# Kernel optimization log

Measured on AMD Instinct MI355X. Metric: run time of the kernel, lower is better.

The kernel has to match this reference:

```python
import jax, jax.numpy as jnp
import numpy as np

B, N, S, F = 16, 512, 7, 256
HID, NUM_CLASSES = 1024, 81
FLAT = S * S * F  # 12544


def setup_inputs() -> dict:
    key = jax.random.key(0)
    ks = jax.random.split(key, 8)
    features = jax.random.normal(ks[0], (B, N, S, S, F), dtype=jnp.float32)
    valid_mask = jax.random.randint(ks[1], (B, N), 0, 2) > 0
    W1 = jax.random.normal(ks[2], (FLAT, HID), dtype=jnp.float32) * (1.0 / np.sqrt(FLAT))
    b1 = jnp.zeros((HID,), dtype=jnp.float32)
    W2 = jax.random.normal(ks[3], (HID, HID), dtype=jnp.float32) * (1.0 / np.sqrt(HID))
    b2 = jnp.zeros((HID,), dtype=jnp.float32)
    W3 = jax.random.normal(ks[4], (HID, NUM_CLASSES), dtype=jnp.float32) * (1.0 / np.sqrt(HID))
    b3 = jnp.zeros((NUM_CLASSES,), dtype=jnp.float32)
    return {"features": features, "valid_mask": valid_mask, "W1": W1, "b1": b1,
            "W2": W2, "b2": b2, "W3": W3, "b3": b3, "features_size_pred": N}


def reference(features, valid_mask, W1, b1, W2, b2, W3, b3, features_size_pred):
    # The TF module masks out invalid ROIs, runs the MLP, then scatters results
    # back to original positions (pad + argsort + gather) with zeros for invalid
    # rows. That is mathematically identical to running the MLP on all ROIs and
    # zeroing invalid rows, which is the efficient dense form.
    b, n = features.shape[0], features.shape[1]
    x = features.reshape(b * n, FLAT)                      # [B*N, 12544]
    h = jax.nn.relu(x @ W1 + b1)                           # [B*N, HID]
    h = jax.nn.relu(h @ W2 + b2)                           # [B*N, HID]
    logits = (h @ W3 + b3).reshape(b, n, NUM_CLASSES)      # [B, N, C]
    mask = valid_mask.astype(logits.dtype)[..., None]      # [B, N, 1]
    return logits * mask
```

## Files before the change

### kernel.cpp

```cpp
#include <hip/hip_runtime.h>
#include <stdint.h>

#define DEVINL __device__ __forceinline__

typedef __bf16 bf16x8 __attribute__((ext_vector_type(8)));
typedef float f32x4 __attribute__((ext_vector_type(4)));

DEVINL unsigned short f32_to_bf16(float f) {
  union { float f; uint32_t u; } v;
  v.f = f;
  uint32_t r = v.u + 0x7fffu + ((v.u >> 16) & 1u);
  return (unsigned short)(r >> 16);
}

DEVINL void load16_to_lds(const void* g, void* l) {
  __builtin_amdgcn_global_load_lds(
      (const __attribute__((address_space(1))) void*)g,
      (__attribute__((address_space(3))) void*)l, 16, 0, 0);
}

__global__ __launch_bounds__(1024) void compact_kernel(
    const int* __restrict__ mask, int* __restrict__ ridx, int* __restrict__ nv) {
  __shared__ int tsum[1024];
  __shared__ int wbase[17];
  const int t = threadIdx.x;
  int flags[8];
  int cnt = 0;
#pragma unroll
  for (int i = 0; i < 8; ++i) {
    flags[i] = (mask[t * 8 + i] != 0) ? 1 : 0;
    cnt += flags[i];
  }
  tsum[t] = cnt;
  __syncthreads();
  if ((t & 63) == 0) {
    int s = 0;
    for (int i = 0; i < 64; ++i) { int v = tsum[t + i]; tsum[t + i] = s; s += v; }
    wbase[t >> 6] = s;
  }
  __syncthreads();
  if (t == 0) {
    int s = 0;
    for (int w = 0; w < 16; ++w) { int v = wbase[w]; wbase[w] = s; s += v; }
    wbase[16] = s;
    *nv = s;
  }
  __syncthreads();
  int base = wbase[t >> 6] + tsum[t];
#pragma unroll
  for (int i = 0; i < 8; ++i)
    if (flags[i]) ridx[base++] = t * 8 + i;
  const int Mv = wbase[16];
  const int Mpad = (Mv + 127) & ~127;
  for (int i = Mv + t; i < Mpad; i += 1024) ridx[i] = 0;
}

__global__ __launch_bounds__(256) void zero_out_kernel(float4* __restrict__ o) {
  o[(size_t)blockIdx.x * 256 + threadIdx.x] = float4{0.f, 0.f, 0.f, 0.f};
}

__global__ __launch_bounds__(256) void gather_cast_kernel(
    const float* __restrict__ feat, const int* __restrict__ ridx,
    const int* __restrict__ nv, unsigned short* __restrict__ out) {
  const int Mpad = ((*nv) + 127) & ~127;
  const unsigned idx = blockIdx.x * 256u + threadIdx.x;
  const unsigned crow = idx / 1568u;
  if ((int)crow >= Mpad) return;
  const int off = (int)(idx - crow * 1568u) * 8;
  const float* src = feat + (size_t)ridx[crow] * 12544 + off;
  float4 a = *reinterpret_cast<const float4*>(src);
  float4 b = *reinterpret_cast<const float4*>(src + 4);
  uint4 p;
  p.x = (uint32_t)f32_to_bf16(a.x) | ((uint32_t)f32_to_bf16(a.y) << 16);
  p.y = (uint32_t)f32_to_bf16(a.z) | ((uint32_t)f32_to_bf16(a.w) << 16);
  p.z = (uint32_t)f32_to_bf16(b.x) | ((uint32_t)f32_to_bf16(b.y) << 16);
  p.w = (uint32_t)f32_to_bf16(b.z) | ((uint32_t)f32_to_bf16(b.w) << 16);
  *reinterpret_cast<uint4*>(out + (size_t)crow * 12544 + off) = p;
}

__global__ void transpose_cast_kernel(const float* __restrict__ W,
                                      unsigned short* __restrict__ Wt,
                                      int K, int Nsrc) {
  __shared__ float tile[32][33];
  const int k0 = blockIdx.x * 32;
  const int n0 = blockIdx.y * 32;
  const int t = threadIdx.x;
#pragma unroll
  for (int i = 0; i < 4; ++i) {
    int idx = t + 256 * i;
    int r = idx >> 5, c = idx & 31;
    int gn = n0 + c;
    float v = (gn < Nsrc) ? W[(size_t)(k0 + r) * Nsrc + gn] : 0.0f;
    tile[r][c] = v;
  }
  __syncthreads();
#pragma unroll
  for (int i = 0; i < 4; ++i) {
    int idx = t + 256 * i;
    int n = idx >> 5, k = idx & 31;
    Wt[(size_t)(n0 + n) * K + (k0 + k)] = f32_to_bf16(tile[k][n]);
  }
}

__global__ __launch_bounds__(256) void reduce_relu_kernel(
    const float* __restrict__ P, const float* __restrict__ bias,
    const int* __restrict__ nv, unsigned short* __restrict__ H) {
  const int Mpad = ((*nv) + 127) & ~127;
  const int m = blockIdx.x;
  if (m >= Mpad) return;
  const int n = threadIdx.x * 4;
  f32x4 s = {};
#pragma unroll
  for (int c = 0; c < 4; ++c) {
    f32x4 v = *reinterpret_cast<const f32x4*>(
        P + ((size_t)c * 8192 + m) * 1024 + n);
    s[0] += v[0]; s[1] += v[1]; s[2] += v[2]; s[3] += v[3];
  }
  f32x4 bv = *reinterpret_cast<const f32x4*>(bias + n);
  uint2 o;
  o.x = (uint32_t)f32_to_bf16(fmaxf(s[0] + bv[0], 0.0f)) |
        ((uint32_t)f32_to_bf16(fmaxf(s[1] + bv[1], 0.0f)) << 16);
  o.y = (uint32_t)f32_to_bf16(fmaxf(s[2] + bv[2], 0.0f)) |
        ((uint32_t)f32_to_bf16(fmaxf(s[3] + bv[3], 0.0f)) << 16);
  *reinterpret_cast<uint2*>(H + (size_t)m * 1024 + n) = o;
}

template <int BM, int BN, bool A_F32, int OMODE>
__global__ __launch_bounds__(256) void gemm_kernel(
    const void* __restrict__ Ap, const unsigned short* __restrict__ Bt,
    const float* __restrict__ bias, unsigned short* __restrict__ Hout,
    float* __restrict__ Fout, const int* __restrict__ ridx,
    const int* __restrict__ nv, int K, int k_len, int Nout, int ldo) {
  constexpr int WM = BM / 32;
  constexpr int WN = BN / 32;
  const int Mv = *nv;
  const int Mpad = (Mv + 127) & ~127;
  const int m0 = blockIdx.y * BM;
  if (m0 >= Mpad) return;

  __shared__ alignas(16) unsigned short As[2][BM * 32];
  __shared__ alignas(16) unsigned short Bs[2][BN * 32];

  const int tid = threadIdx.x;
  const int wave = tid >> 6, lane = tid & 63;
  const int wm = wave >> 1, wn = wave & 1;
  const int n0 = blockIdx.x * BN;
  const int ks = blockIdx.z * k_len;
  const int ke = ks + k_len;

  const float* Af = (const float*)Ap;
  const unsigned short* Ab = (const unsigned short*)Ap;

  f32x4 acc[WM][WN] = {};

  auto stage = [&](int b, int k0) {
    if constexpr (A_F32) {
      constexpr int NF4 = (BM * 32) / (256 * 4);
#pragma unroll
      for (int i = 0; i < NF4; ++i) {
        int idx = tid + 256 * i;
        int r = idx >> 3, c4 = idx & 7;
        float4 v = *reinterpret_cast<const float4*>(
            Af + (size_t)ridx[m0 + r] * K + (k0 + c4 * 4));
        uint2 p;
        p.x = (uint32_t)f32_to_bf16(v.x) | ((uint32_t)f32_to_bf16(v.y) << 16);
        p.y = (uint32_t)f32_to_bf16(v.z) | ((uint32_t)f32_to_bf16(v.w) << 16);
        *reinterpret_cast<uint2*>(&As[b][r * 32 + c4 * 4]) = p;
      }
    } else {
#pragma unroll
      for (int c = wave; c < BM / 16; c += 4) {
        int row = c * 16 + (lane >> 2);
        load16_to_lds(Ab + (size_t)(m0 + row) * K + (k0 + (lane & 3) * 8),
                      &As[b][c * 512]);
      }
    }
#pragma unroll
    for (int c = wave; c < BN / 16; c += 4) {
      int row = c * 16 + (lane >> 2);
      load16_to_lds(Bt + (size_t)(n0 + row) * K + (k0 + (lane & 3) * 8),
                    &Bs[b][c * 512]);
    }
  };

  auto compute = [&](int b) {
    bf16x8 a[WM], bb[WN];
#pragma unroll
    for (int i = 0; i < WM; ++i)
      a[i] = *reinterpret_cast<const bf16x8*>(
          &As[b][(wm * WM * 16 + i * 16 + (lane & 15)) * 32 + (lane >> 4) * 8]);
#pragma unroll
    for (int j = 0; j < WN; ++j)
      bb[j] = *reinterpret_cast<const bf16x8*>(
          &Bs[b][(wn * WN * 16 + j * 16 + (lane & 15)) * 32 + (lane >> 4) * 8]);
#pragma unroll
    for (int i = 0; i < WM; ++i)
#pragma unroll
      for (int j = 0; j < WN; ++j)
        acc[i][j] = __builtin_amdgcn_mfma_f32_16x16x32_bf16(a[i], bb[j],
                                                            acc[i][j], 0, 0, 0);
  };

  stage(0, ks);
  __syncthreads();
  int cur = 0;
  for (int k0 = ks + 32; k0 < ke; k0 += 32) {
    stage(cur ^ 1, k0);
    compute(cur);
    __syncthreads();
    cur ^= 1;
  }
  compute(cur);

  const int l15 = lane & 15, quad = lane >> 4;
#pragma unroll
  for (int j = 0; j < WN; ++j) {
    int n = n0 + wn * WN * 16 + j * 16 + l15;
    if (n >= Nout) continue;
    float bn = (OMODE == 2) ? 0.0f : bias[n];
#pragma unroll
    for (int i = 0; i < WM; ++i) {
      int mb = m0 + wm * WM * 16 + i * 16 + quad * 4;
      f32x4 v = acc[i][j];
#pragma unroll
      for (int r = 0; r < 4; ++r) {
        int m = mb + r;
        if constexpr (OMODE == 0) {
          Hout[(size_t)m * ldo + n] = f32_to_bf16(fmaxf(v[r] + bn, 0.0f));
        } else if constexpr (OMODE == 1) {
          if (m < Mv) Fout[(size_t)ridx[m] * ldo + n] = v[r] + bn;
        } else {
          Fout[((size_t)blockIdx.z * 8192 + m) * (size_t)ldo + n] = v[r];
        }
      }
    }
  }
}

extern "C" void kernel_launch(void* const* d_in, const int* in_sizes, int n_in,
                              void* d_out, int out_size, void* d_ws,
                              size_t ws_size, hipStream_t stream) {
  const float* feat = (const float*)d_in[0];
  const int* mask = (const int*)d_in[1];
  const float* W1 = (const float*)d_in[2];
  const float* b1 = (const float*)d_in[3];
  const float* W2 = (const float*)d_in[4];
  const float* b2 = (const float*)d_in[5];
  const float* W3 = (const float*)d_in[6];
  const float* b3 = (const float*)d_in[7];
  float* out = (float*)d_out;

  char* ws = (char*)d_ws;
  size_t off = 0;
  int* ridx = (int*)(ws + off); off += 32768;
  int* nv   = (int*)(ws + off); off += 256;
  unsigned short* W1t = (unsigned short*)(ws + off); off += 25690112;
  unsigned short* W2t = (unsigned short*)(ws + off); off += 2097152;
  unsigned short* W3t = (unsigned short*)(ws + off); off += 196608;
  unsigned short* H1  = (unsigned short*)(ws + off); off += 16777216;
  unsigned short* H2  = (unsigned short*)(ws + off); off += 16777216;
  unsigned short* Fb  = (unsigned short*)(ws + off); off += 205520896;
  size_t need_base = off;
  float* P = (float*)(ws + off); off += 134217728;
  size_t need_split = off;

  compact_kernel<<<1, 1024, 0, stream>>>(mask, ridx, nv);
  zero_out_kernel<<<648, 256, 0, stream>>>((float4*)out);
  transpose_cast_kernel<<<dim3(392, 32), 256, 0, stream>>>(W1, W1t, 12544, 1024);
  transpose_cast_kernel<<<dim3(32, 32), 256, 0, stream>>>(W2, W2t, 1024, 1024);
  transpose_cast_kernel<<<dim3(32, 3), 256, 0, stream>>>(W3, W3t, 1024, 81);

  if (ws_size >= need_split) {
    gather_cast_kernel<<<50176, 256, 0, stream>>>(feat, ridx, nv, Fb);
    gemm_kernel<128, 128, false, 2><<<dim3(8, 64, 4), 256, 0, stream>>>(
        Fb, W1t, b1, nullptr, P, ridx, nv, 12544, 3136, 1024, 1024);
    reduce_relu_kernel<<<8192, 256, 0, stream>>>(P, b1, nv, H1);
  } else if (ws_size >= need_base) {
    gather_cast_kernel<<<50176, 256, 0, stream>>>(feat, ridx, nv, Fb);
    gemm_kernel<128, 128, false, 0><<<dim3(8, 64, 1), 256, 0, stream>>>(
        Fb, W1t, b1, H1, nullptr, ridx, nv, 12544, 12544, 1024, 1024);
  } else {
    gemm_kernel<128, 128, true, 0><<<dim3(8, 64, 1), 256, 0, stream>>>(
        feat, W1t, b1, H1, nullptr, ridx, nv, 12544, 12544, 1024, 1024);
  }
  gemm_kernel<128, 128, false, 0><<<dim3(8, 64, 1), 256, 0, stream>>>(
      H1, W2t, b2, H2, nullptr, ridx, nv, 1024, 1024, 1024, 1024);
  gemm_kernel<32, 96, false, 1><<<dim3(1, 256, 1), 256, 0, stream>>>(
      H2, W3t, b3, nullptr, out, ridx, nv, 1024, 1024, 81, 81);
}
```

Before: 836.5 us.

## Fuse gather and bf16 cast into layer-1 GEMM with register-prefetched A staging

Removes the separate gather_cast pass and its large bf16 staging buffer. The layer-1 split-K GEMM now reads fp32 feature rows through the compacted row index and converts them to bf16 while staging into LDS. The global loads are issued before compute and written to LDS after it, so the load latency is hidden. The change also adds a block-index swizzle so blocks that share an N-tile run together, sets launch bounds to 4 blocks per SM, and moves the layer-2 GEMM to 64-row tiles. The risks are more register pressure and uncoalesced fp32 row gathers inside the GEMM.

```diff
diff --git a/kernel.cpp b/kernel.cpp
--- a/kernel.cpp
+++ b/kernel.cpp
@@ -57,25 +57,6 @@
 
 __global__ __launch_bounds__(256) void zero_out_kernel(float4* __restrict__ o) {
   o[(size_t)blockIdx.x * 256 + threadIdx.x] = float4{0.f, 0.f, 0.f, 0.f};
-}
-
-__global__ __launch_bounds__(256) void gather_cast_kernel(
-    const float* __restrict__ feat, const int* __restrict__ ridx,
-    const int* __restrict__ nv, unsigned short* __restrict__ out) {
-  const int Mpad = ((*nv) + 127) & ~127;
-  const unsigned idx = blockIdx.x * 256u + threadIdx.x;
-  const unsigned crow = idx / 1568u;
-  if ((int)crow >= Mpad) return;
-  const int off = (int)(idx - crow * 1568u) * 8;
-  const float* src = feat + (size_t)ridx[crow] * 12544 + off;
-  float4 a = *reinterpret_cast<const float4*>(src);
-  float4 b = *reinterpret_cast<const float4*>(src + 4);
-  uint4 p;
-  p.x = (uint32_t)f32_to_bf16(a.x) | ((uint32_t)f32_to_bf16(a.y) << 16);
-  p.y = (uint32_t)f32_to_bf16(a.z) | ((uint32_t)f32_to_bf16(a.w) << 16);
-  p.z = (uint32_t)f32_to_bf16(b.x) | ((uint32_t)f32_to_bf16(b.y) << 16);
-  p.w = (uint32_t)f32_to_bf16(b.z) | ((uint32_t)f32_to_bf16(b.w) << 16);
-  *reinterpret_cast<uint4*>(out + (size_t)crow * 12544 + off) = p;
 }
 
 __global__ void transpose_cast_kernel(const float* __restrict__ W,
@@ -125,17 +106,25 @@
   *reinterpret_cast<uint2*>(H + (size_t)m * 1024 + n) = o;
 }
 
-template <int BM, int BN, bool A_F32, int OMODE>
-__global__ __launch_bounds__(256) void gemm_kernel(
+template <int BM, int BN, bool A_F32, int OMODE, bool SWZ>
+__global__ __launch_bounds__(256, 4) void gemm_kernel(
     const void* __restrict__ Ap, const unsigned short* __restrict__ Bt,
     const float* __restrict__ bias, unsigned short* __restrict__ Hout,
     float* __restrict__ Fout, const int* __restrict__ ridx,
     const int* __restrict__ nv, int K, int k_len, int Nout, int ldo) {
   constexpr int WM = BM / 32;
   constexpr int WN = BN / 32;
+  int bx, by, bz;
+  if constexpr (SWZ) {
+    int orig = blockIdx.x + ((blockIdx.y + (blockIdx.z << 6)) << 3);
+    int swz = ((orig & 7) << 8) | (orig >> 3);
+    by = swz & 63; bx = (swz >> 6) & 7; bz = swz >> 9;
+  } else {
+    bx = blockIdx.x; by = blockIdx.y; bz = blockIdx.z;
+  }
   const int Mv = *nv;
   const int Mpad = (Mv + 127) & ~127;
-  const int m0 = blockIdx.y * BM;
+  const int m0 = by * BM;
   if (m0 >= Mpad) return;
 
   __shared__ alignas(16) unsigned short As[2][BM * 32];
@@ -144,8 +133,8 @@
   const int tid = threadIdx.x;
   const int wave = tid >> 6, lane = tid & 63;
   const int wm = wave >> 1, wn = wave & 1;
-  const int n0 = blockIdx.x * BN;
-  const int ks = blockIdx.z * k_len;
+  const int n0 = bx * BN;
+  const int ks = bz * k_len;
   const int ke = ks + k_len;
 
   const float* Af = (const float*)Ap;
@@ -153,28 +142,40 @@
 
   f32x4 acc[WM][WN] = {};
 
-  auto stage = [&](int b, int k0) {
-    if constexpr (A_F32) {
-      constexpr int NF4 = (BM * 32) / (256 * 4);
-#pragma unroll
-      for (int i = 0; i < NF4; ++i) {
-        int idx = tid + 256 * i;
-        int r = idx >> 3, c4 = idx & 7;
-        float4 v = *reinterpret_cast<const float4*>(
-            Af + (size_t)ridx[m0 + r] * K + (k0 + c4 * 4));
-        uint2 p;
-        p.x = (uint32_t)f32_to_bf16(v.x) | ((uint32_t)f32_to_bf16(v.y) << 16);
-        p.y = (uint32_t)f32_to_bf16(v.z) | ((uint32_t)f32_to_bf16(v.w) << 16);
-        *reinterpret_cast<uint2*>(&As[b][r * 32 + c4 * 4]) = p;
-      }
-    } else {
-#pragma unroll
-      for (int c = wave; c < BM / 16; c += 4) {
-        int row = c * 16 + (lane >> 2);
-        load16_to_lds(Ab + (size_t)(m0 + row) * K + (k0 + (lane & 3) * 8),
-                      &As[b][c * 512]);
-      }
-    }
+  const float* aptr[4];
+  if constexpr (A_F32) {
+    static_assert(BM == 128, "fp32 A staging assumes BM=128");
+#pragma unroll
+    for (int i = 0; i < 4; ++i) {
+      int r = (tid >> 3) + 32 * i;
+      aptr[i] = Af + (size_t)ridx[m0 + r] * K + (tid & 7) * 4;
+    }
+  }
+
+  auto loadA_f32 = [&](int k0, float4* va) {
+#pragma unroll
+    for (int i = 0; i < 4; ++i)
+      va[i] = *reinterpret_cast<const float4*>(aptr[i] + k0);
+  };
+  auto writeA_f32 = [&](int b, const float4* va) {
+#pragma unroll
+    for (int i = 0; i < 4; ++i) {
+      int r = (tid >> 3) + 32 * i, c4 = tid & 7;
+      uint2 p;
+      p.x = (uint32_t)f32_to_bf16(va[i].x) | ((uint32_t)f32_to_bf16(va[i].y) << 16);
+      p.y = (uint32_t)f32_to_bf16(va[i].z) | ((uint32_t)f32_to_bf16(va[i].w) << 16);
+      *reinterpret_cast<uint2*>(&As[b][r * 32 + c4 * 4]) = p;
+    }
+  };
+  auto stageA_async = [&](int b, int k0) {
+#pragma unroll
+    for (int c = wave; c < BM / 16; c += 4) {
+      int row = c * 16 + (lane >> 2);
+      load16_to_lds(Ab + (size_t)(m0 + row) * K + (k0 + (lane & 3) * 8),
+                    &As[b][c * 512]);
+    }
+  };
+  auto stageB = [&](int b, int k0) {
 #pragma unroll
     for (int c = wave; c < BN / 16; c += 4) {
       int row = c * 16 + (lane >> 2);
@@ -201,12 +202,17 @@
                                                             acc[i][j], 0, 0, 0);
   };
 
-  stage(0, ks);
+  float4 va[4];
+  if constexpr (A_F32) loadA_f32(ks, va); else stageA_async(0, ks);
+  stageB(0, ks);
+  if constexpr (A_F32) writeA_f32(0, va);
   __syncthreads();
   int cur = 0;
   for (int k0 = ks + 32; k0 < ke; k0 += 32) {
-    stage(cur ^ 1, k0);
+    if constexpr (A_F32) loadA_f32(k0, va); else stageA_async(cur ^ 1, k0);
+    stageB(cur ^ 1, k0);
     compute(cur);
+    if constexpr (A_F32) writeA_f32(cur ^ 1, va);
     __syncthreads();
     cur ^= 1;
   }
@@ -230,7 +236,7 @@
         } else if constexpr (OMODE == 1) {
           if (m < Mv) Fout[(size_t)ridx[m] * ldo + n] = v[r] + bn;
         } else {
-          Fout[((size_t)blockIdx.z * 8192 + m) * (size_t)ldo + n] = v[r];
+          Fout[((size_t)bz * 8192 + m) * (size_t)ldo + n] = v[r];
         }
       }
     }
@@ -259,7 +265,6 @@
   unsigned short* W3t = (unsigned short*)(ws + off); off += 196608;
   unsigned short* H1  = (unsigned short*)(ws + off); off += 16777216;
   unsigned short* H2  = (unsigned short*)(ws + off); off += 16777216;
-  unsigned short* Fb  = (unsigned short*)(ws + off); off += 205520896;
   size_t need_base = off;
   float* P = (float*)(ws + off); off += 134217728;
   size_t need_split = off;
@@ -271,20 +276,15 @@
   transpose_cast_kernel<<<dim3(32, 3), 256, 0, stream>>>(W3, W3t, 1024, 81);
 
   if (ws_size >= need_split) {
-    gather_cast_kernel<<<50176, 256, 0, stream>>>(feat, ridx, nv, Fb);
-    gemm_kernel<128, 128, false, 2><<<dim3(8, 64, 4), 256, 0, stream>>>(
-        Fb, W1t, b1, nullptr, P, ridx, nv, 12544, 3136, 1024, 1024);
+    gemm_kernel<128, 128, true, 2, true><<<dim3(8, 64, 4), 256, 0, stream>>>(
+        feat, W1t, b1, nullptr, P, ridx, nv, 12544, 3136, 1024, 1024);
     reduce_relu_kernel<<<8192, 256, 0, stream>>>(P, b1, nv, H1);
-  } else if (ws_size >= need_base) {
-    gather_cast_kernel<<<50176, 256, 0, stream>>>(feat, ridx, nv, Fb);
-    gemm_kernel<128, 128, false, 0><<<dim3(8, 64, 1), 256, 0, stream>>>(
-        Fb, W1t, b1, H1, nullptr, ridx, nv, 12544, 12544, 1024, 1024);
   } else {
-    gemm_kernel<128, 128, true, 0><<<dim3(8, 64, 1), 256, 0, stream>>>(
+    gemm_kernel<128, 128, true, 0, false><<<dim3(8, 64, 1), 256, 0, stream>>>(
         feat, W1t, b1, H1, nullptr, ridx, nv, 12544, 12544, 1024, 1024);
   }
-  gemm_kernel<128, 128, false, 0><<<dim3(8, 64, 1), 256, 0, stream>>>(
+  gemm_kernel<64, 128, false, 0, false><<<dim3(8, 128, 1), 256, 0, stream>>>(
       H1, W2t, b2, H2, nullptr, ridx, nv, 1024, 1024, 1024, 1024);
-  gemm_kernel<32, 96, false, 1><<<dim3(1, 256, 1), 256, 0, stream>>>(
+  gemm_kernel<32, 96, false, 1, false><<<dim3(1, 256, 1), 256, 0, stream>>>(
       H2, W3t, b3, nullptr, out, ridx, nv, 1024, 1024, 81, 81);
 }
```

Result: faster. 816.7 us (-2.4%).
